# Kernel tuning notes

Hardware: AMD Instinct MI355X
Metric: run time of the kernel (lower is better)

The kernel has to match this reference:

```python
import jax, jax.numpy as jnp
import numpy as np

B, T, N, D = 4, 24, 2048, 128
H = 4
HD = D // H
E = 8
K = 2
INTER = 512            # dim * mlp_ratio
MINTER = INTER // K    # per-expert intermediate (512//2 = 256)
EPS = 1e-6
ALPHA = 0.05           # GCN residual mixing
SCALE = HD ** -0.5


def setup_inputs() -> dict:
    key = jax.random.key(0)
    ks = jax.random.split(key, 32)
    w = lambda i, shape: (jax.random.normal(ks[i], shape, jnp.float32) * 0.02)
    inp = {
        "x": jax.random.normal(ks[0], (B, T, N, D), jnp.float32),
        "k": jax.random.normal(ks[1], (B, T, N, D), jnp.float32),
        "v": jax.random.normal(ks[2], (B, T, N, D), jnp.float32),
        "adj": jax.random.uniform(ks[3], (N, N), jnp.float32),
        # attention qkv projections (torch Linear: y = x @ W.T + b)
        "Wq": w(4, (D, D)), "bq": jnp.zeros((D,), jnp.float32),
        "Wk": w(5, (D, D)), "bk": jnp.zeros((D,), jnp.float32),
        "Wv": w(6, (D, D)), "bv": jnp.zeros((D,), jnp.float32),
        "norm_tatt_w": jnp.ones((D,), jnp.float32),
        # GCN
        "gcn_fc1_w": w(7, (D, D)),
        "gcn_mlp_w": w(8, (D, D)), "gcn_mlp_b": jnp.zeros((D,), jnp.float32),
        # block norms
        "norm1_w": jnp.ones((D,), jnp.float32),
        "norm2_w": jnp.ones((D,), jnp.float32),
        # MoE
        "gate_w": w(9, (E, D)),
        "ew1": w(10, (E, MINTER, D)),
        "ew2": w(11, (E, D, MINTER)),
        "ew3": w(12, (E, MINTER, D)),
        "sw1": w(13, (INTER, D)),
        "sw2": w(14, (D, INTER)),
        "sw3": w(15, (INTER, D)),
        "sgate_w": w(16, (1, D)),
    }
    return inp


def rms_norm(x, w):
    var = jnp.mean(x * x, axis=-1, keepdims=True)
    return w * (x * jax.lax.rsqrt(var + EPS))


def swiglu(x, w1, w2, w3):
    return (jax.nn.silu(x @ w1.T) * (x @ w3.T)) @ w2.T


def reference(x, k, v, adj, Wq, bq, Wk, bk, Wv, bv, norm_tatt_w,
              gcn_fc1_w, gcn_mlp_w, gcn_mlp_b, norm1_w, norm2_w,
              gate_w, ew1, ew2, ew3, sw1, sw2, sw3, sgate_w):
    # ---- pre-norm ----
    x_n = rms_norm(x, norm1_w)
    k_n = rms_norm(k, norm1_w)

    # ---- temporal self-attention (per node, over T) ----
    def heads(y, W, b):  # [B,T,N,D] -> [B,N,H,T,hd]
        y = y @ W.T + b
        return y.transpose(0, 2, 1, 3).reshape(B, N, -1, H, HD).transpose(0, 1, 3, 2, 4)

    q = heads(x_n, Wq, bq)
    kk = heads(k_n, Wk, bk)
    vv = heads(k_n, Wv, bv)  # module passes k for both k and v
    attn = jnp.einsum('bnhqd,bnhkd->bnhqk', q, kk) * SCALE
    attn = jax.nn.softmax(attn, axis=-1)
    t_x = jnp.einsum('bnhqk,bnhkd->bnhqd', attn, vv)
    t_x = t_x.transpose(0, 3, 1, 2, 4).reshape(B, T, N, D)  # [B,T,N,D]
    t_x = rms_norm(t_x, norm_tatt_w)

    # ---- GCN: row-normalized adjacency over node axis ----
    a = adj / jnp.sum(adj, axis=1, keepdims=True)            # a[n,k] = adj[n,k]/d[n]
    mixed = jnp.einsum('nk,btkd->btnd', a, t_x)
    gcn_out = mixed @ gcn_fc1_w.T
    out = ALPHA * t_x + (1.0 - ALPHA) * gcn_out
    ho = out @ gcn_mlp_w.T + gcn_mlp_b

    x = x + ho  # residual (drop_path = identity)

    # ---- MoE sparse experts ----
    x2 = rms_norm(x, norm2_w).reshape(-1, D)                 # [Tok, D]
    router_logits = x2 @ gate_w.T                            # [Tok, E]
    rw = jax.nn.softmax(router_logits.astype(jnp.float32), axis=-1)
    top_w, top_idx = jax.lax.top_k(rw, K)                    # [Tok, K]
    top_w = top_w.astype(x2.dtype)

    final = jnp.zeros_like(x2)
    for e in range(E):  # fixed small expert count
        coef = jnp.sum(jnp.where(top_idx == e, top_w, 0.0), axis=-1)  # [Tok]
        final = final + coef[:, None] * swiglu(x2, ew1[e], ew2[e], ew3[e])

    shared = swiglu(x2, sw1, sw2, sw3)
    shared = jax.nn.sigmoid(x2 @ sgate_w.T) * shared
    final = final + shared

    x = x + final.reshape(B, T, N, D)
    return x, router_logits
```

## Files before the change

kernel.cpp:

```cpp
#include <hip/hip_runtime.h>

#define BB 4
#define TT 24
#define NN 2048
#define DD 128
#define HH 4
#define HD 32
#define TOK 196608
#define EE 8
#define MINTER 256
#define INTER 512

typedef unsigned short u16;
typedef __attribute__((ext_vector_type(8))) short  bf16x8;
typedef __attribute__((ext_vector_type(4))) float  f32x4;
typedef __attribute__((ext_vector_type(4))) unsigned int u32x4;

#define MFMA(a,b,c) __builtin_amdgcn_mfma_f32_16x16x32_bf16((a),(b),(c),0,0,0)
#define AS(n) __attribute__((address_space(n)))

static __device__ __forceinline__ u16 f2b(float f) {
    union { float f; unsigned u; } v; v.f = f;
    unsigned r = v.u + 0x7FFFu + ((v.u >> 16) & 1u);
    return (u16)(r >> 16);
}
static __device__ __forceinline__ float b2f(u16 b) {
    union { unsigned u; float f; } v; v.u = ((unsigned)b) << 16;
    return v.f;
}
static __device__ __forceinline__ float silu_mul(float u, float v) {
    return u * __builtin_amdgcn_rcpf(1.f + __expf(-u)) * v;
}

template<int C>
static __device__ __forceinline__ bf16x8 frag_ld(const u16* s, int row, int kbyte) {
    constexpr int mask = ((C/8) < 8 ? (C/8) : 8) - 1;
    int byte = row * (C * 2) + (kbyte ^ ((row & mask) << 4));
    return *(const bf16x8*)((const char*)s + byte);
}
template<int C>
static __device__ __forceinline__ u16 lds_us(const u16* s, int r, int c) {
    constexpr int mask = ((C/8) < 8 ? (C/8) : 8) - 1;
    int byte = r * (C * 2) + ((((c >> 3) << 4) ^ ((r & mask) << 4))) + ((c & 7) << 1);
    return *(const u16*)((const char*)s + byte);
}
template<int C>
static __device__ __forceinline__ void lds_store_us(u16* s, int r, int c, u16 v) {
    constexpr int mask = ((C/8) < 8 ? (C/8) : 8) - 1;
    int byte = r * (C * 2) + ((((c >> 3) << 4) ^ ((r & mask) << 4))) + ((c & 7) << 1);
    *(u16*)((char*)s + byte) = v;
}
template<int C>
static __device__ __forceinline__ void stage_bf16(u16* s, const u16* g, int gstride,
                                                  int rows, int tid, int nthr) {
    constexpr int cpr = C / 8;
    constexpr int mask = (cpr < 8 ? cpr : 8) - 1;
    for (int i = tid; i < rows * cpr; i += nthr) {
        int r = i / cpr, cc = i - r * cpr;
        u32x4 v = *(const u32x4*)(g + (size_t)r * gstride + cc * 8);
        *(u32x4*)((char*)s + r * (C * 2) + ((cc * 16) ^ ((r & mask) << 4))) = v;
    }
}
static __device__ __forceinline__ void stage_async64(u16* s, const u16* g, int wi, int lane) {
    int slot = wi * 64 + lane;
    int r = slot >> 3, c = slot & 7;
    const u16* src = g + r * 2048 + ((c ^ (r & 7)) << 3);
    __builtin_amdgcn_global_load_lds((const AS(1) void*)src,
                                     (AS(3) void*)(s + wi * 512), 16, 0, 0);
}
static __device__ __forceinline__ void zero_acc(f32x4 acc[4][4]) {
    f32x4 z = {0.f, 0.f, 0.f, 0.f};
    #pragma unroll
    for (int i = 0; i < 4; ++i)
        #pragma unroll
        for (int j = 0; j < 4; ++j) acc[i][j] = z;
}
template<int CA, int CB>
static __device__ __forceinline__ void gemm_step64(const u16* sA, const u16* sB,
        int arow0, int brow0, int kbyte, f32x4 acc[4][4], int ln15) {
    bf16x8 a[4], b[4];
    #pragma unroll
    for (int i = 0; i < 4; ++i) a[i] = frag_ld<CA>(sA, arow0 + i * 16 + ln15, kbyte);
    #pragma unroll
    for (int j = 0; j < 4; ++j) b[j] = frag_ld<CB>(sB, brow0 + j * 16 + ln15, kbyte);
    #pragma unroll
    for (int i = 0; i < 4; ++i)
        #pragma unroll
        for (int j = 0; j < 4; ++j)
            acc[i][j] = MFMA(a[i], b[j], acc[i][j]);
}

static __device__ __forceinline__ void prefetch_regs(u32x4 pf[6],
        const u16* __restrict__ w1b, const u16* __restrict__ w3b,
        const u16* __restrict__ w2b, int w2s, int tid) {
    #pragma unroll
    for (int p = 0; p < 6; ++p) {
        int i = p * 256 + tid;
        const u16* src;
        if (i < 512)       { int r = i >> 4, cc = i & 15; src = w1b + r * 128 + cc * 8; }
        else if (i < 1024) { int j = i - 512; int r = j >> 4, cc = j & 15; src = w3b + r * 128 + cc * 8; }
        else               { int j = i - 1024; int r = j >> 2, cc = j & 3; src = w2b + (size_t)r * w2s + cc * 8; }
        pf[p] = *(const u32x4*)src;
    }
}
static __device__ __forceinline__ void write_chunk(u16* buf, const u32x4 pf[6], int tid) {
    #pragma unroll
    for (int p = 0; p < 6; ++p) {
        int i = p * 256 + tid;
        char* dst;
        if (i < 512)       { int r = i >> 4, cc = i & 15; dst = (char*)buf + r * 256 + ((cc * 16) ^ ((r & 7) << 4)); }
        else if (i < 1024) { int j = i - 512; int r = j >> 4, cc = j & 15; dst = (char*)(buf + 4096) + r * 256 + ((cc * 16) ^ ((r & 7) << 4)); }
        else               { int j = i - 1024; int r = j >> 2, cc = j & 3; dst = (char*)(buf + 8192) + r * 64 + ((cc * 16) ^ ((r & 3) << 4)); }
        *(u32x4*)dst = pf[p];
    }
}
static __device__ __forceinline__ void swiglu_chunk(const u16* buf, u16* sH,
        const bf16x8 av[2][4], f32x4 aout[2][8],
        int wid, int g16, int ln15) {
    const u16* W1c = buf;
    const u16* W3c = buf + 4096;
    const u16* W2c = buf + 8192;
    f32x4 z = {0.f, 0.f, 0.f, 0.f};
    f32x4 a1[2][2], a3[2][2];
    #pragma unroll
    for (int mf = 0; mf < 2; ++mf)
        #pragma unroll
        for (int nf = 0; nf < 2; ++nf) { a1[mf][nf] = z; a3[mf][nf] = z; }
    #pragma unroll
    for (int ks = 0; ks < 4; ++ks) {
        int kb = ks * 64 + g16 * 16;
        #pragma unroll
        for (int nf = 0; nf < 2; ++nf) {
            bf16x8 b1 = frag_ld<128>(W1c, nf * 16 + ln15, kb);
            bf16x8 b3 = frag_ld<128>(W3c, nf * 16 + ln15, kb);
            a1[0][nf] = MFMA(av[0][ks], b1, a1[0][nf]);
            a1[1][nf] = MFMA(av[1][ks], b1, a1[1][nf]);
            a3[0][nf] = MFMA(av[0][ks], b3, a3[0][nf]);
            a3[1][nf] = MFMA(av[1][ks], b3, a3[1][nf]);
        }
    }
    #pragma unroll
    for (int mf = 0; mf < 2; ++mf)
        #pragma unroll
        for (int nf = 0; nf < 2; ++nf)
            #pragma unroll
            for (int r = 0; r < 4; ++r) {
                int row = wid * 32 + mf * 16 + g16 * 4 + r;
                int col = nf * 16 + ln15;
                lds_store_us<32>(sH, row, col, f2b(silu_mul(a1[mf][nf][r], a3[mf][nf][r])));
            }
    asm volatile("s_waitcnt lgkmcnt(0)" ::: "memory");
    __builtin_amdgcn_sched_barrier(0);
    {
        int kb = g16 * 16;
        bf16x8 ah0 = frag_ld<32>(sH, wid * 32 + ln15, kb);
        bf16x8 ah1 = frag_ld<32>(sH, wid * 32 + 16 + ln15, kb);
        #pragma unroll
        for (int nf = 0; nf < 8; ++nf) {
            bf16x8 bw = frag_ld<32>(W2c, nf * 16 + ln15, kb);
            aout[0][nf] = MFMA(ah0, bw, aout[0][nf]);
            aout[1][nf] = MFMA(ah1, bw, aout[1][nf]);
        }
    }
}

__global__ __launch_bounds__(256) void preconvert(
        const float* __restrict__ Wq, const float* __restrict__ Wk,
        const float* __restrict__ Wv, const float* __restrict__ g1,
        const float* __restrict__ g2,
        const float* __restrict__ e1, const float* __restrict__ e2,
        const float* __restrict__ e3,
        const float* __restrict__ s1, const float* __restrict__ s2,
        const float* __restrict__ s3,
        u16* __restrict__ arena, int* __restrict__ cnts) {
    int idx = blockIdx.x * 256 + threadIdx.x;
    if (blockIdx.x == 0 && threadIdx.x < 8) cnts[threadIdx.x] = 0;
    if (idx >= 266240) return;
    const float* src; int rel;
    if (idx < 20480) {
        int s = idx >> 12; rel = idx & 4095;
        src = (s == 0) ? Wq : (s == 1) ? Wk : (s == 2) ? Wv : (s == 3) ? g1 : g2;
    } else if (idx < 217088) {
        int t = idx - 20480; int s = t >> 16; rel = t & 65535;
        src = (s == 0) ? e1 : (s == 1) ? e2 : e3;
    } else {
        int t = idx - 217088; int s = t >> 14; rel = t & 16383;
        src = (s == 0) ? s1 : (s == 1) ? s2 : s3;
    }
    const float4 v = *(const float4*)(src + (size_t)rel * 4);
    union { unsigned long long q; u16 us[4]; } o;
    o.us[0] = f2b(v.x); o.us[1] = f2b(v.y); o.us[2] = f2b(v.z); o.us[3] = f2b(v.w);
    *(unsigned long long*)(arena + (size_t)idx * 4) = o.q;
}

__global__ __launch_bounds__(256) void rmsnorm_pair(
        const float* __restrict__ x, const float* __restrict__ k,
        const float* __restrict__ w, u16* __restrict__ xn, u16* __restrict__ kn) {
    int row = blockIdx.x * 4 + (threadIdx.x >> 6);
    int lane = threadIdx.x & 63;
    const float* in; u16* out;
    if (row < TOK) { in = x + (size_t)row * 128; out = xn + (size_t)row * 128; }
    else           { in = k + (size_t)(row - TOK) * 128; out = kn + (size_t)(row - TOK) * 128; }
    float2 v = *(const float2*)(in + lane * 2);
    float ss = v.x * v.x + v.y * v.y;
    #pragma unroll
    for (int o = 32; o > 0; o >>= 1) ss += __shfl_xor(ss, o);
    float sc = rsqrtf(ss * (1.f / 128.f) + 1e-6f);
    float2 wv = *(const float2*)(w + lane * 2);
    unsigned pack = ((unsigned)f2b(v.y * sc * wv.y) << 16) | (unsigned)f2b(v.x * sc * wv.x);
    *(unsigned*)(out + lane * 2) = pack;
}

__global__ __launch_bounds__(256) void proj128(
        const u16* __restrict__ in, const u16* __restrict__ W,
        const float* __restrict__ bias, u16* __restrict__ out) {
    int tok0 = blockIdx.x * 128;
    __shared__ u16 sA[128 * 128];
    __shared__ u16 sW[128 * 128];
    int tid = threadIdx.x, lane = tid & 63, ln15 = lane & 15, g16 = lane >> 4, wid = tid >> 6;
    int wm = (wid >> 1) * 64, wn = (wid & 1) * 64;
    stage_bf16<128>(sA, in + (size_t)tok0 * 128, 128, 128, tid, 256);
    stage_bf16<128>(sW, W, 128, 128, tid, 256);
    __syncthreads();
    f32x4 acc[4][4];
    zero_acc(acc);
    #pragma unroll
    for (int ks = 0; ks < 4; ++ks)
        gemm_step64<128, 128>(sA, sW, wm, wn, ks * 64 + g16 * 16, acc, ln15);
    #pragma unroll
    for (int j = 0; j < 4; ++j) {
        int col = wn + j * 16 + ln15;
        float bv = bias[col];
        #pragma unroll
        for (int i = 0; i < 4; ++i)
            #pragma unroll
            for (int r = 0; r < 4; ++r) {
                int row = wm + i * 16 + g16 * 4 + r;
                out[(size_t)(tok0 + row) * 128 + col] = f2b(acc[i][j][r] + bv);
            }
    }
}

__global__ __launch_bounds__(256) void attn_kernel(
        const u16* __restrict__ q, const u16* __restrict__ kk, const u16* __restrict__ vv,
        const float* __restrict__ ntw, u16* __restrict__ txn) {
    int bid = blockIdx.x;
    int b = bid >> 11;
    int n = bid & 2047;
    __shared__ u16 sQ[4][24][32];
    __shared__ u16 sK[4][24][32];
    __shared__ u16 sV[4][24][32];
    __shared__ float sS[4][24][24];
    __shared__ float sO[24][128];
    int tid = threadIdx.x, lane = tid & 63, wid = tid >> 6;
    for (int idx = tid; idx < 3072; idx += 256) {
        int h = idx / 768;
        int rem = idx - h * 768;
        int t = rem >> 5;
        int d = rem & 31;
        size_t off = ((size_t)((b * 24 + t) * 2048 + n)) * 128 + h * 32 + d;
        sQ[h][t][d] = q[off];
        sK[h][t][d] = kk[off];
        sV[h][t][d] = vv[off];
    }
    __syncthreads();
    int h = wid;
    for (int i = lane; i < 576; i += 64) {
        int qi = i / 24, ki = i - qi * 24;
        float s = 0.f;
        #pragma unroll
        for (int c = 0; c < 32; ++c) s += b2f(sQ[h][qi][c]) * b2f(sK[h][ki][c]);
        sS[h][qi][ki] = s * 0.17677669529663687f;
    }
    __syncthreads();
    if (lane < 24) {
        float m = -1e30f;
        #pragma unroll
        for (int c = 0; c < 24; ++c) m = fmaxf(m, sS[h][lane][c]);
        float e[24]; float sum = 0.f;
        #pragma unroll
        for (int c = 0; c < 24; ++c) { e[c] = __expf(sS[h][lane][c] - m); sum += e[c]; }
        float inv = 1.f / sum;
        #pragma unroll
        for (int c = 0; c < 24; ++c) sS[h][lane][c] = e[c] * inv;
    }
    __syncthreads();
    for (int i = lane; i < 768; i += 64) {
        int qi = i >> 5, d = i & 31;
        float acc = 0.f;
        #pragma unroll
        for (int c = 0; c < 24; ++c) acc += sS[h][qi][c] * b2f(sV[h][c][d]);
        sO[qi][h * 32 + d] = acc;
    }
    __syncthreads();
    for (int j = 0; j < 6; ++j) {
        int t = wid * 6 + j;
        float v0 = sO[t][lane], v1 = sO[t][lane + 64];
        float ss = v0 * v0 + v1 * v1;
        #pragma unroll
        for (int o = 32; o > 0; o >>= 1) ss += __shfl_xor(ss, o);
        float sc = rsqrtf(ss * (1.f / 128.f) + 1e-6f);
        size_t off = ((size_t)((b * 24 + t) * 2048 + n)) * 128;
        txn[off + lane]      = f2b(v0 * sc * ntw[lane]);
        txn[off + lane + 64] = f2b(v1 * sc * ntw[lane + 64]);
    }
}

__global__ __launch_bounds__(256) void adj_norm(const float* __restrict__ adj, u16* __restrict__ abf) {
    int nrow = blockIdx.x;
    const float* r = adj + (size_t)nrow * 2048;
    int tid = threadIdx.x;
    float s = 0.f;
    for (int c = tid; c < 2048; c += 256) s += r[c];
    __shared__ float red[4];
    #pragma unroll
    for (int o = 32; o > 0; o >>= 1) s += __shfl_xor(s, o);
    if ((tid & 63) == 0) red[tid >> 6] = s;
    __syncthreads();
    float inv = 1.f / (red[0] + red[1] + red[2] + red[3]);
    u16* o = abf + (size_t)nrow * 2048;
    for (int c = tid; c < 2048; c += 256) o[c] = f2b(r[c] * inv);
}

__global__ __launch_bounds__(256) void transpose_k(const u16* __restrict__ txn, u16* __restrict__ txT) {
    int bt = blockIdx.x >> 5;
    int n0 = (blockIdx.x & 31) * 64;
    int tid = threadIdx.x;
    int nn = tid & 63, dg = tid >> 6;
    for (int rep = 0; rep < 4; ++rep) {
        int d0 = rep * 32 + dg * 8;
        union { u32x4 v; u16 us[8]; } u;
        u.v = *(const u32x4*)(txn + ((size_t)(bt * 2048 + n0 + nn)) * 128 + d0);
        #pragma unroll
        for (int j = 0; j < 8; ++j)
            txT[((size_t)(bt * 128 + d0 + j)) * 2048 + n0 + nn] = u.us[j];
    }
}

__global__ __launch_bounds__(256) void gcn_gemm(
        const u16* __restrict__ abf, const u16* __restrict__ txT, u16* __restrict__ mixed) {
    int bt = blockIdx.x >> 4;
    int n0 = (blockIdx.x & 15) * 128;
    __shared__ u16 sA[128 * 64];
    __shared__ u16 sB[128 * 64];
    int tid = threadIdx.x, lane = tid & 63, ln15 = lane & 15, g16 = lane >> 4, wid = tid >> 6;
    int wm = (wid >> 1) * 64, wn = (wid & 1) * 64;
    f32x4 acc[4][4];
    zero_acc(acc);
    const u16* aRow = abf + (size_t)n0 * 2048;
    const u16* bRow = txT + (size_t)bt * 128 * 2048;
    for (int k0 = 0; k0 < 2048; k0 += 64) {
        __syncthreads();
        #pragma unroll
        for (int i = 0; i < 4; ++i) stage_async64(sA, aRow + k0, wid * 4 + i, lane);
        #pragma unroll
        for (int i = 0; i < 4; ++i) stage_async64(sB, bRow + k0, wid * 4 + i, lane);
        __syncthreads();
        #pragma unroll
        for (int ks = 0; ks < 2; ++ks)
            gemm_step64<64, 64>(sA, sB, wm, wn, ks * 64 + g16 * 16, acc, ln15);
    }
    u16* out = mixed + ((size_t)(bt * 2048 + n0)) * 128;
    #pragma unroll
    for (int i = 0; i < 4; ++i)
        #pragma unroll
        for (int j = 0; j < 4; ++j)
            #pragma unroll
            for (int r = 0; r < 4; ++r) {
                int row = wm + i * 16 + g16 * 4 + r;
                int col = wn + j * 16 + ln15;
                out[(size_t)row * 128 + col] = f2b(acc[i][j][r]);
            }
}

__global__ __launch_bounds__(256) void fused_gcn_router(
        const u16* __restrict__ mixed, const u16* __restrict__ txn,
        const float* __restrict__ x,
        const u16* __restrict__ W1, const u16* __restrict__ W2,
        const float* __restrict__ bias2, const float* __restrict__ n2w,
        const float* __restrict__ gatew,
        float* __restrict__ outx, float* __restrict__ outlog,
        u16* __restrict__ x2n,
        int* __restrict__ lists, float* __restrict__ listw, int* __restrict__ cnts) {
    int tok0 = blockIdx.x * 128;
    __shared__ char LB[65536];
    __shared__ float sGate[1024];
    __shared__ float sN2[128];
    __shared__ float sBias[128];
    __shared__ float sLog[1024];
    __shared__ float sPart[256];
    __shared__ float sScale[128];
    __shared__ int sBCnt[8];
    __shared__ int sGBase[8];
    u16* sM = (u16*)LB;
    u16* sW = (u16*)(LB + 32768);
    float* sXn = (float*)LB;
    int tid = threadIdx.x, lane = tid & 63, ln15 = lane & 15, g16 = lane >> 4, wid = tid >> 6;
    int wm = (wid >> 1) * 64, wn = (wid & 1) * 64;
    stage_bf16<128>(sM, mixed + (size_t)tok0 * 128, 128, 128, tid, 256);
    stage_bf16<128>(sW, W1, 128, 128, tid, 256);
    for (int i = tid; i < 1024; i += 256) sGate[i] = gatew[i];
    if (tid < 128) { sN2[tid] = n2w[tid]; sBias[tid] = bias2[tid]; }
    if (tid < 8) sBCnt[tid] = 0;
    __syncthreads();
    f32x4 acc[4][4];
    zero_acc(acc);
    #pragma unroll
    for (int ks = 0; ks < 4; ++ks)
        gemm_step64<128, 128>(sM, sW, wm, wn, ks * 64 + g16 * 16, acc, ln15);
    __syncthreads();
    stage_bf16<128>(sM, txn + (size_t)tok0 * 128, 128, 128, tid, 256);
    stage_bf16<128>(sW, W2, 128, 128, tid, 256);
    __syncthreads();
    #pragma unroll
    for (int i = 0; i < 4; ++i)
        #pragma unroll
        for (int j = 0; j < 4; ++j)
            #pragma unroll
            for (int r = 0; r < 4; ++r) {
                int row = wm + i * 16 + g16 * 4 + r;
                int col = wn + j * 16 + ln15;
                float tv = b2f(lds_us<128>(sM, row, col));
                lds_store_us<128>(sM, row, col, f2b(0.05f * tv + 0.95f * acc[i][j][r]));
            }
    __syncthreads();
    zero_acc(acc);
    #pragma unroll
    for (int ks = 0; ks < 4; ++ks)
        gemm_step64<128, 128>(sM, sW, wm, wn, ks * 64 + g16 * 16, acc, ln15);
    #pragma unroll
    for (int i = 0; i < 4; ++i)
        #pragma unroll
        for (int j = 0; j < 4; ++j)
            #pragma unroll
            for (int r = 0; r < 4; ++r) {
                int row = wm + i * 16 + g16 * 4 + r;
                int col = wn + j * 16 + ln15;
                float xv = x[(size_t)(tok0 + row) * 128 + col] + acc[i][j][r] + sBias[col];
                outx[(size_t)(tok0 + row) * 128 + col] = xv;
                acc[i][j][r] = xv;
            }
    #pragma unroll
    for (int i = 0; i < 4; ++i)
        #pragma unroll
        for (int r = 0; r < 4; ++r) {
            float s = 0.f;
            #pragma unroll
            for (int j = 0; j < 4; ++j) s += acc[i][j][r] * acc[i][j][r];
            s += __shfl_xor(s, 1); s += __shfl_xor(s, 2);
            s += __shfl_xor(s, 4); s += __shfl_xor(s, 8);
            if (ln15 == 0) sPart[(wm + i * 16 + g16 * 4 + r) * 2 + (wid & 1)] = s;
        }
    __syncthreads();
    if (tid < 128)
        sScale[tid] = rsqrtf((sPart[tid * 2] + sPart[tid * 2 + 1]) * (1.f / 128.f) + 1e-6f);
    __syncthreads();
    #pragma unroll
    for (int i = 0; i < 4; ++i)
        #pragma unroll
        for (int j = 0; j < 4; ++j)
            #pragma unroll
            for (int r = 0; r < 4; ++r) {
                int row = wm + i * 16 + g16 * 4 + r;
                int col = wn + j * 16 + ln15;
                sXn[row * 128 + col] = acc[i][j][r] * sScale[row] * sN2[col];
            }
    __syncthreads();
    {
        int r = tid >> 1, e0 = (tid & 1) * 4;
        float a0 = 0, a1 = 0, a2 = 0, a3 = 0;
        for (int cc = 0; cc < 128; ++cc) {
            int c = (cc + r) & 127;
            float v = sXn[r * 128 + c];
            a0 += v * sGate[(e0 + 0) * 128 + c];
            a1 += v * sGate[(e0 + 1) * 128 + c];
            a2 += v * sGate[(e0 + 2) * 128 + c];
            a3 += v * sGate[(e0 + 3) * 128 + c];
        }
        int rb = r * 8 + e0;
        sLog[rb + 0] = a0; sLog[rb + 1] = a1; sLog[rb + 2] = a2; sLog[rb + 3] = a3;
        size_t ob = (size_t)(tok0 + r) * 8 + e0;
        outlog[ob + 0] = a0; outlog[ob + 1] = a1; outlog[ob + 2] = a2; outlog[ob + 3] = a3;
    }
    for (int cc = tid; cc < 2048; cc += 256) {
        int r = cc >> 4, c0 = (cc & 15) * 8;
        union { u32x4 v; u16 us[8]; } u;
        #pragma unroll
        for (int jj = 0; jj < 8; ++jj) u.us[jj] = f2b(sXn[r * 128 + c0 + jj]);
        *(u32x4*)(x2n + (size_t)(tok0 + r) * 128 + c0) = u.v;
    }
    __syncthreads();
    int e1 = 0, e2 = 0, le1 = 0, le2 = 0;
    float w1v = 0.f, w2v = 0.f;
    if (tid < 128) {
        int r = tid;
        float l[8];
        #pragma unroll
        for (int e = 0; e < 8; ++e) l[e] = sLog[r * 8 + e];
        float m = l[0];
        #pragma unroll
        for (int e = 1; e < 8; ++e) m = fmaxf(m, l[e]);
        float ex[8]; float s = 0.f;
        #pragma unroll
        for (int e = 0; e < 8; ++e) { ex[e] = __expf(l[e] - m); s += ex[e]; }
        float inv = 1.f / s;
        float b1v = ex[0]; e1 = 0;
        #pragma unroll
        for (int e = 1; e < 8; ++e) if (ex[e] > b1v) { b1v = ex[e]; e1 = e; }
        e2 = (e1 == 0) ? 1 : 0; float b2v = ex[e2];
        #pragma unroll
        for (int e = 0; e < 8; ++e) if (e != e1 && ex[e] > b2v) { b2v = ex[e]; e2 = e; }
        w1v = b1v * inv; w2v = b2v * inv;
        le1 = atomicAdd(&sBCnt[e1], 1);
        le2 = atomicAdd(&sBCnt[e2], 1);
    }
    __syncthreads();
    if (tid < 8) sGBase[tid] = atomicAdd(&cnts[tid], sBCnt[tid]);
    __syncthreads();
    if (tid < 128) {
        int tok = tok0 + tid;
        int p1 = sGBase[e1] + le1;
        lists[(size_t)e1 * TOK + p1] = tok * 2 + 0; listw[(size_t)e1 * TOK + p1] = w1v;
        int p2 = sGBase[e2] + le2;
        lists[(size_t)e2 * TOK + p2] = tok * 2 + 1; listw[(size_t)e2 * TOK + p2] = w2v;
    }
}

__global__ __launch_bounds__(256, 2) void moe_expert(
        const u16* __restrict__ x2n, const int* __restrict__ lists,
        const float* __restrict__ listw, const int* __restrict__ cnts,
        const u16* __restrict__ bw1, const u16* __restrict__ bw2,
        const u16* __restrict__ bw3, u16* __restrict__ slotOut) {
    int e = blockIdx.y;
    int base = blockIdx.x * 128;
    int cnt = cnts[e];
    if (base >= cnt) return;
    int valid = min(128, cnt - base);
    const int* lst = lists + (size_t)e * TOK + base;
    const float* lw = listw + (size_t)e * TOK + base;
    __shared__ u16 sX2[128 * 128];
    __shared__ u16 sBufA[12288];
    __shared__ u16 sH[128 * 32];
    __shared__ float sCoef[128];
    __shared__ int sTok[128];
    u16* bufB = sX2;
    int tid = threadIdx.x, lane = tid & 63, ln15 = lane & 15, g16 = lane >> 4, wid = tid >> 6;
    if (tid < 128) {
        int t = (tid < valid) ? lst[tid] : -1;
        sTok[tid] = t;
        sCoef[tid] = (tid < valid) ? lw[tid] : 0.f;
    }
    const u16* w1base = bw1 + (size_t)e * (256 * 128);
    const u16* w3base = bw3 + (size_t)e * (256 * 128);
    const u16* w2base = bw2 + (size_t)e * (128 * 256);
    u32x4 pf0[6];
    prefetch_regs(pf0, w1base, w3base, w2base, 256, tid);
    __syncthreads();
    for (int i = tid; i < 2048; i += 256) {
        int r = i >> 4, cc = i & 15;
        int t = sTok[r];
        u32x4 v = {0, 0, 0, 0};
        if (t >= 0) v = *(const u32x4*)(x2n + (size_t)(t >> 1) * 128 + cc * 8);
        *(u32x4*)((char*)sX2 + r * 256 + ((cc * 16) ^ ((r & 7) << 4))) = v;
    }
    write_chunk(sBufA, pf0, tid);
    __syncthreads();
    bf16x8 av[2][4];
    #pragma unroll
    for (int mf = 0; mf < 2; ++mf)
        #pragma unroll
        for (int ks = 0; ks < 4; ++ks)
            av[mf][ks] = frag_ld<128>(sX2, wid * 32 + mf * 16 + ln15, ks * 64 + g16 * 16);
    f32x4 aout[2][8];
    f32x4 z = {0.f, 0.f, 0.f, 0.f};
    #pragma unroll
    for (int mf = 0; mf < 2; ++mf)
        #pragma unroll
        for (int nf = 0; nf < 8; ++nf) aout[mf][nf] = z;
    __syncthreads();
    for (int ic = 0; ic < 8; ++ic) {
        u16* cur = (ic & 1) ? bufB : sBufA;
        u16* alt = (ic & 1) ? sBufA : bufB;
        u32x4 pf[6];
        bool hasNext = (ic + 1 < 8);
        if (hasNext)
            prefetch_regs(pf, w1base + (ic + 1) * 4096, w3base + (ic + 1) * 4096,
                          w2base + (ic + 1) * 32, 256, tid);
        swiglu_chunk(cur, sH, av, aout, wid, g16, ln15);
        if (hasNext) write_chunk(alt, pf, tid);
        __syncthreads();
    }
    #pragma unroll
    for (int mf = 0; mf < 2; ++mf)
        #pragma unroll
        for (int nf = 0; nf < 8; ++nf)
            #pragma unroll
            for (int r = 0; r < 4; ++r) {
                int row = wid * 32 + mf * 16 + g16 * 4 + r;
                if (row < valid) {
                    int col = nf * 16 + ln15;
                    slotOut[(size_t)sTok[row] * 128 + col] = f2b(sCoef[row] * aout[mf][nf][r]);
                }
            }
}

__global__ __launch_bounds__(256, 2) void moe_shared(
        const u16* __restrict__ x2n, const u16* __restrict__ bw1,
        const u16* __restrict__ bw2, const u16* __restrict__ bw3,
        const float* __restrict__ sgw, const u16* __restrict__ slotOut,
        float* __restrict__ outx) {
    int tok0 = blockIdx.x * 128;
    __shared__ u16 sX2[128 * 128];
    __shared__ u16 sBufA[12288];
    __shared__ u16 sH[128 * 32];
    __shared__ float sGv[128];
    __shared__ float sSG[128];
    u16* bufB = sX2;
    int tid = threadIdx.x, lane = tid & 63, ln15 = lane & 15, g16 = lane >> 4, wid = tid >> 6;
    u32x4 pf0[6];
    prefetch_regs(pf0, bw1, bw3, bw2, 512, tid);
    stage_bf16<128>(sX2, x2n + (size_t)tok0 * 128, 128, 128, tid, 256);
    write_chunk(sBufA, pf0, tid);
    if (tid < 128) sSG[tid] = sgw[tid];
    __syncthreads();
    if (tid < 128) {
        float d = 0.f;
        for (int cc = 0; cc < 128; ++cc) {
            int c = (cc + tid) & 127;
            d += b2f(lds_us<128>(sX2, tid, c)) * sSG[c];
        }
        sGv[tid] = 1.f / (1.f + __expf(-d));
    }
    bf16x8 av[2][4];
    #pragma unroll
    for (int mf = 0; mf < 2; ++mf)
        #pragma unroll
        for (int ks = 0; ks < 4; ++ks)
            av[mf][ks] = frag_ld<128>(sX2, wid * 32 + mf * 16 + ln15, ks * 64 + g16 * 16);
    f32x4 aout[2][8];
    f32x4 z = {0.f, 0.f, 0.f, 0.f};
    #pragma unroll
    for (int mf = 0; mf < 2; ++mf)
        #pragma unroll
        for (int nf = 0; nf < 8; ++nf) aout[mf][nf] = z;
    __syncthreads();
    for (int ic = 0; ic < 16; ++ic) {
        u16* cur = (ic & 1) ? bufB : sBufA;
        u16* alt = (ic & 1) ? sBufA : bufB;
        u32x4 pf[6];
        bool hasNext = (ic + 1 < 16);
        if (hasNext)
            prefetch_regs(pf, bw1 + (ic + 1) * 4096, bw3 + (ic + 1) * 4096,
                          bw2 + (ic + 1) * 32, 512, tid);
        swiglu_chunk(cur, sH, av, aout, wid, g16, ln15);
        if (hasNext) write_chunk(alt, pf, tid);
        __syncthreads();
    }
    #pragma unroll
    for (int mf = 0; mf < 2; ++mf)
        #pragma unroll
        for (int nf = 0; nf < 8; ++nf)
            #pragma unroll
            for (int r = 0; r < 4; ++r) {
                int row = wid * 32 + mf * 16 + g16 * 4 + r;
                int col = nf * 16 + ln15;
                size_t t = (size_t)(tok0 + row);
                float fc = b2f(slotOut[(t * 2 + 0) * 128 + col])
                         + b2f(slotOut[(t * 2 + 1) * 128 + col]);
                size_t idx = t * 128 + col;
                outx[idx] = outx[idx] + fc + sGv[row] * aout[mf][nf][r];
            }
}

#define SZTD  ((size_t)TOK * 128 * 2)
#define OFF_XN   ((size_t)0)
#define OFF_KN   (SZTD)
#define OFF_Q    (SZTD * 2)
#define OFF_KP   (SZTD * 3)
#define OFF_VP   (SZTD * 4)
#define OFF_ABF  (SZTD * 5)
#define OFF_LW   (OFF_ABF + 8388608)
#define OFF_LIST (OFF_LW + (size_t)8 * TOK * 4)
#define OFF_CNT  (OFF_LIST + (size_t)8 * TOK * 4)
#define OFF_ARENA (OFF_CNT + 128)

extern "C" void kernel_launch(void* const* d_in, const int* in_sizes, int n_in,
                              void* d_out, int out_size, void* d_ws, size_t ws_size,
                              hipStream_t stream) {
    (void)in_sizes; (void)n_in; (void)out_size; (void)ws_size;
    const float* x    = (const float*)d_in[0];
    const float* k    = (const float*)d_in[1];
    const float* adj  = (const float*)d_in[3];
    const float* Wq   = (const float*)d_in[4];
    const float* bq   = (const float*)d_in[5];
    const float* Wk   = (const float*)d_in[6];
    const float* bk   = (const float*)d_in[7];
    const float* Wv   = (const float*)d_in[8];
    const float* bv   = (const float*)d_in[9];
    const float* ntw  = (const float*)d_in[10];
    const float* gfc1 = (const float*)d_in[11];
    const float* gmlp = (const float*)d_in[12];
    const float* gmlpb= (const float*)d_in[13];
    const float* n1w  = (const float*)d_in[14];
    const float* n2w  = (const float*)d_in[15];
    const float* gatew= (const float*)d_in[16];
    const float* ew1  = (const float*)d_in[17];
    const float* ew2  = (const float*)d_in[18];
    const float* ew3  = (const float*)d_in[19];
    const float* sw1  = (const float*)d_in[20];
    const float* sw2  = (const float*)d_in[21];
    const float* sw3  = (const float*)d_in[22];
    const float* sgw  = (const float*)d_in[23];

    char* ws = (char*)d_ws;
    u16*  xn   = (u16*)(ws + OFF_XN);
    u16*  kn   = (u16*)(ws + OFF_KN);
    u16*  qb   = (u16*)(ws + OFF_Q);
    u16*  kpb  = (u16*)(ws + OFF_KP);
    u16*  vpb  = (u16*)(ws + OFF_VP);
    u16*  slotOut = (u16*)(ws + OFF_KP);
    u16*  abf  = (u16*)(ws + OFF_ABF);
    float* lw  = (float*)(ws + OFF_LW);
    int*  lst  = (int*)(ws + OFF_LIST);
    int*  cnts = (int*)(ws + OFF_CNT);
    u16*  arena = (u16*)(ws + OFF_ARENA);
    u16*  bWq = arena;
    u16*  bWk = arena + 16384;
    u16*  bWv = arena + 32768;
    u16*  bG1 = arena + 49152;
    u16*  bG2 = arena + 65536;
    u16*  bE1 = arena + 81920;
    u16*  bE2 = arena + 344064;
    u16*  bE3 = arena + 606208;
    u16*  bS1 = arena + 868352;
    u16*  bS2 = arena + 933888;
    u16*  bS3 = arena + 999424;
    float* outx   = (float*)d_out;
    float* outlog = outx + (size_t)TOK * 128;

    preconvert<<<1040, 256, 0, stream>>>(Wq, Wk, Wv, gfc1, gmlp, ew1, ew2, ew3,
                                         sw1, sw2, sw3, arena, cnts);
    rmsnorm_pair<<<98304, 256, 0, stream>>>(x, k, n1w, xn, kn);
    proj128<<<1536, 256, 0, stream>>>(xn, bWq, bq, qb);
    proj128<<<1536, 256, 0, stream>>>(kn, bWk, bk, kpb);
    proj128<<<1536, 256, 0, stream>>>(kn, bWv, bv, vpb);
    attn_kernel<<<8192, 256, 0, stream>>>(qb, kpb, vpb, ntw, xn );
    adj_norm<<<2048, 256, 0, stream>>>(adj, abf);
    transpose_k<<<3072, 256, 0, stream>>>(xn, qb );
    gcn_gemm<<<1536, 256, 0, stream>>>(abf, qb, kn );
    fused_gcn_router<<<1536, 256, 0, stream>>>(kn, xn, x, bG1, bG2, gmlpb, n2w, gatew,
                                               outx, outlog, qb , lst, lw, cnts);
    moe_expert<<<dim3(1536, 8), 256, 0, stream>>>(qb, lst, lw, cnts, bE1, bE2, bE3, slotOut);
    moe_shared<<<1536, 256, 0, stream>>>(qb, bS1, bS2, bS3, sgw, slotOut, outx);
}
```

Measured before the change: 779.8 us.

## Shrink MoE kernel LDS to single buffer and raise occupancy to three blocks

```diff
diff --git a/kernel.cpp b/kernel.cpp
--- a/kernel.cpp
+++ b/kernel.cpp
@@ -50,6 +50,12 @@
     int byte = r * (C * 2) + ((((c >> 3) << 4) ^ ((r & mask) << 4))) + ((c & 7) << 1);
     *(u16*)((char*)s + byte) = v;
 }
+static __device__ __forceinline__ bf16x8 frag_ld_p80(const u16* s, int row, int kbyte) {
+    return *(const bf16x8*)((const char*)s + row * 80 + kbyte);
+}
+static __device__ __forceinline__ void sh_store_p80(u16* s, int r, int c, u16 v) {
+    *(u16*)((char*)s + r * 80 + c * 2) = v;
+}
 template<int C>
 static __device__ __forceinline__ void stage_bf16(u16* s, const u16* g, int gstride,
                                                   int rows, int tid, int nthr) {
@@ -109,8 +115,8 @@
         int i = p * 256 + tid;
         char* dst;
         if (i < 512)       { int r = i >> 4, cc = i & 15; dst = (char*)buf + r * 256 + ((cc * 16) ^ ((r & 7) << 4)); }
-        else if (i < 1024) { int j = i - 512; int r = j >> 4, cc = j & 15; dst = (char*)(buf + 4096) + r * 256 + ((cc * 16) ^ ((r & 7) << 4)); }
-        else               { int j = i - 1024; int r = j >> 2, cc = j & 3; dst = (char*)(buf + 8192) + r * 64 + ((cc * 16) ^ ((r & 3) << 4)); }
+        else if (i < 1024) { int j = i - 512; int r = j >> 4, cc = j & 15; dst = (char*)buf + 8192 + r * 256 + ((cc * 16) ^ ((r & 7) << 4)); }
+        else               { int j = i - 1024; int r = j >> 2, cc = j & 3; dst = (char*)buf + 16384 + r * 80 + cc * 16; }
         *(u32x4*)dst = pf[p];
     }
 }
@@ -147,17 +153,17 @@
             for (int r = 0; r < 4; ++r) {
                 int row = wid * 32 + mf * 16 + g16 * 4 + r;
                 int col = nf * 16 + ln15;
-                lds_store_us<32>(sH, row, col, f2b(silu_mul(a1[mf][nf][r], a3[mf][nf][r])));
+                sh_store_p80(sH, row, col, f2b(silu_mul(a1[mf][nf][r], a3[mf][nf][r])));
             }
     asm volatile("s_waitcnt lgkmcnt(0)" ::: "memory");
     __builtin_amdgcn_sched_barrier(0);
     {
         int kb = g16 * 16;
-        bf16x8 ah0 = frag_ld<32>(sH, wid * 32 + ln15, kb);
-        bf16x8 ah1 = frag_ld<32>(sH, wid * 32 + 16 + ln15, kb);
+        bf16x8 ah0 = frag_ld_p80(sH, wid * 32 + ln15, kb);
+        bf16x8 ah1 = frag_ld_p80(sH, wid * 32 + 16 + ln15, kb);
         #pragma unroll
         for (int nf = 0; nf < 8; ++nf) {
-            bf16x8 bw = frag_ld<32>(W2c, nf * 16 + ln15, kb);
+            bf16x8 bw = frag_ld_p80(W2c, nf * 16 + ln15, kb);
             aout[0][nf] = MFMA(ah0, bw, aout[0][nf]);
             aout[1][nf] = MFMA(ah1, bw, aout[1][nf]);
         }
@@ -526,7 +532,7 @@
     }
 }
 
-__global__ __launch_bounds__(256, 2) void moe_expert(
+__global__ __launch_bounds__(256, 3) void moe_expert(
         const u16* __restrict__ x2n, const int* __restrict__ lists,
         const float* __restrict__ listw, const int* __restrict__ cnts,
         const u16* __restrict__ bw1, const u16* __restrict__ bw2,
@@ -538,12 +544,10 @@
     int valid = min(128, cnt - base);
     const int* lst = lists + (size_t)e * TOK + base;
     const float* lw = listw + (size_t)e * TOK + base;
-    __shared__ u16 sX2[128 * 128];
-    __shared__ u16 sBufA[12288];
-    __shared__ u16 sH[128 * 32];
+    __shared__ u16 sBuf[13312];
+    __shared__ u16 sH[5120];
     __shared__ float sCoef[128];
     __shared__ int sTok[128];
-    u16* bufB = sX2;
     int tid = threadIdx.x, lane = tid & 63, ln15 = lane & 15, g16 = lane >> 4, wid = tid >> 6;
     if (tid < 128) {
         int t = (tid < valid) ? lst[tid] : -1;
@@ -556,39 +560,39 @@
     u32x4 pf0[6];
     prefetch_regs(pf0, w1base, w3base, w2base, 256, tid);
     __syncthreads();
-    for (int i = tid; i < 2048; i += 256) {
-        int r = i >> 4, cc = i & 15;
-        int t = sTok[r];
-        u32x4 v = {0, 0, 0, 0};
-        if (t >= 0) v = *(const u32x4*)(x2n + (size_t)(t >> 1) * 128 + cc * 8);
-        *(u32x4*)((char*)sX2 + r * 256 + ((cc * 16) ^ ((r & 7) << 4))) = v;
-    }
-    write_chunk(sBufA, pf0, tid);
-    __syncthreads();
     bf16x8 av[2][4];
-    #pragma unroll
-    for (int mf = 0; mf < 2; ++mf)
-        #pragma unroll
-        for (int ks = 0; ks < 4; ++ks)
-            av[mf][ks] = frag_ld<128>(sX2, wid * 32 + mf * 16 + ln15, ks * 64 + g16 * 16);
+    {
+        bf16x8 zz = {0, 0, 0, 0, 0, 0, 0, 0};
+        int t0 = sTok[wid * 32 + ln15];
+        int t1 = sTok[wid * 32 + 16 + ln15];
+        const u16* r0 = x2n + (size_t)(t0 >> 1) * 128;
+        const u16* r1 = x2n + (size_t)(t1 >> 1) * 128;
+        #pragma unroll
+        for (int ks = 0; ks < 4; ++ks) {
+            av[0][ks] = (t0 >= 0) ? *(const bf16x8*)(r0 + ks * 32 + g16 * 8) : zz;
+            av[1][ks] = (t1 >= 0) ? *(const bf16x8*)(r1 + ks * 32 + g16 * 8) : zz;
+        }
+    }
+    write_chunk(sBuf, pf0, tid);
+    __syncthreads();
     f32x4 aout[2][8];
     f32x4 z = {0.f, 0.f, 0.f, 0.f};
     #pragma unroll
     for (int mf = 0; mf < 2; ++mf)
         #pragma unroll
         for (int nf = 0; nf < 8; ++nf) aout[mf][nf] = z;
-    __syncthreads();
     for (int ic = 0; ic < 8; ++ic) {
-        u16* cur = (ic & 1) ? bufB : sBufA;
-        u16* alt = (ic & 1) ? sBufA : bufB;
         u32x4 pf[6];
         bool hasNext = (ic + 1 < 8);
         if (hasNext)
             prefetch_regs(pf, w1base + (ic + 1) * 4096, w3base + (ic + 1) * 4096,
                           w2base + (ic + 1) * 32, 256, tid);
-        swiglu_chunk(cur, sH, av, aout, wid, g16, ln15);
-        if (hasNext) write_chunk(alt, pf, tid);
-        __syncthreads();
+        swiglu_chunk(sBuf, sH, av, aout, wid, g16, ln15);
+        if (hasNext) {
+            __syncthreads();
+            write_chunk(sBuf, pf, tid);
+            __syncthreads();
+        }
     }
     #pragma unroll
     for (int mf = 0; mf < 2; ++mf)
@@ -604,57 +608,59 @@
             }
 }
 
-__global__ __launch_bounds__(256, 2) void moe_shared(
+__global__ __launch_bounds__(256, 3) void moe_shared(
         const u16* __restrict__ x2n, const u16* __restrict__ bw1,
         const u16* __restrict__ bw2, const u16* __restrict__ bw3,
         const float* __restrict__ sgw, const u16* __restrict__ slotOut,
         float* __restrict__ outx) {
     int tok0 = blockIdx.x * 128;
-    __shared__ u16 sX2[128 * 128];
-    __shared__ u16 sBufA[12288];
-    __shared__ u16 sH[128 * 32];
+    __shared__ u16 sBuf[13312];
+    __shared__ u16 sH[5120];
     __shared__ float sGv[128];
-    __shared__ float sSG[128];
-    u16* bufB = sX2;
     int tid = threadIdx.x, lane = tid & 63, ln15 = lane & 15, g16 = lane >> 4, wid = tid >> 6;
     u32x4 pf0[6];
     prefetch_regs(pf0, bw1, bw3, bw2, 512, tid);
-    stage_bf16<128>(sX2, x2n + (size_t)tok0 * 128, 128, 128, tid, 256);
-    write_chunk(sBufA, pf0, tid);
-    if (tid < 128) sSG[tid] = sgw[tid];
-    __syncthreads();
+    bf16x8 av[2][4];
+    {
+        const u16* r0 = x2n + (size_t)(tok0 + wid * 32 + ln15) * 128;
+        const u16* r1 = x2n + (size_t)(tok0 + wid * 32 + 16 + ln15) * 128;
+        #pragma unroll
+        for (int ks = 0; ks < 4; ++ks) {
+            av[0][ks] = *(const bf16x8*)(r0 + ks * 32 + g16 * 8);
+            av[1][ks] = *(const bf16x8*)(r1 + ks * 32 + g16 * 8);
+        }
+    }
     if (tid < 128) {
+        const u16* xr = x2n + (size_t)(tok0 + tid) * 128;
         float d = 0.f;
-        for (int cc = 0; cc < 128; ++cc) {
-            int c = (cc + tid) & 127;
-            d += b2f(lds_us<128>(sX2, tid, c)) * sSG[c];
+        #pragma unroll
+        for (int c8 = 0; c8 < 16; ++c8) {
+            bf16x8 v = *(const bf16x8*)(xr + c8 * 8);
+            #pragma unroll
+            for (int j = 0; j < 8; ++j) d += b2f((u16)v[j]) * sgw[c8 * 8 + j];
         }
         sGv[tid] = 1.f / (1.f + __expf(-d));
     }
-    bf16x8 av[2][4];
-    #pragma unroll
-    for (int mf = 0; mf < 2; ++mf)
-        #pragma unroll
-        for (int ks = 0; ks < 4; ++ks)
-            av[mf][ks] = frag_ld<128>(sX2, wid * 32 + mf * 16 + ln15, ks * 64 + g16 * 16);
+    write_chunk(sBuf, pf0, tid);
+    __syncthreads();
     f32x4 aout[2][8];
     f32x4 z = {0.f, 0.f, 0.f, 0.f};
     #pragma unroll
     for (int mf = 0; mf < 2; ++mf)
         #pragma unroll
         for (int nf = 0; nf < 8; ++nf) aout[mf][nf] = z;
-    __syncthreads();
     for (int ic = 0; ic < 16; ++ic) {
-        u16* cur = (ic & 1) ? bufB : sBufA;
-        u16* alt = (ic & 1) ? sBufA : bufB;
         u32x4 pf[6];
         bool hasNext = (ic + 1 < 16);
         if (hasNext)
             prefetch_regs(pf, bw1 + (ic + 1) * 4096, bw3 + (ic + 1) * 4096,
                           bw2 + (ic + 1) * 32, 512, tid);
-        swiglu_chunk(cur, sH, av, aout, wid, g16, ln15);
-        if (hasNext) write_chunk(alt, pf, tid);
-        __syncthreads();
+        swiglu_chunk(sBuf, sH, av, aout, wid, g16, ln15);
+        if (hasNext) {
+            __syncthreads();
+            write_chunk(sBuf, pf, tid);
+            __syncthreads();
+        }
     }
     #pragma unroll
     for (int mf = 0; mf < 2; ++mf)
```

New measurement: 1.114 ms. 42.9% more time.
